# Optimization experiments

Measured on AMD Instinct MI355X. Metric: run time of the kernel, lower is better.

Reference implementation:

```python
import jax, jax.numpy as jnp
import numpy as np

N_NODES = 50000
N_EDGES = 600000
D_IN = 128
HIDDEN = 128
N_CLASSES = 2
BN_EPS = 1e-5


def setup_inputs() -> dict:
    key = jax.random.key(0)
    ks = jax.random.split(key, 10)
    x = jax.random.normal(ks[0], (N_NODES, D_IN), dtype=jnp.float32)
    edge_index = jax.random.randint(ks[1], (2, N_EDGES), 0, N_NODES, dtype=jnp.int64)
    # weights stored [in, out] (transpose of torch Linear.weight)
    s1 = 1.0 / np.sqrt(D_IN)
    s2 = 1.0 / np.sqrt(HIDDEN)
    W1 = jax.random.uniform(ks[2], (D_IN, HIDDEN), jnp.float32, -s1, s1)
    b1 = jax.random.uniform(ks[3], (HIDDEN,), jnp.float32, -s1, s1)
    gamma = jnp.ones((HIDDEN,), jnp.float32)
    beta = jnp.zeros((HIDDEN,), jnp.float32)
    W2 = jax.random.uniform(ks[4], (HIDDEN, HIDDEN), jnp.float32, -s2, s2)
    b2 = jax.random.uniform(ks[5], (HIDDEN,), jnp.float32, -s2, s2)
    Wl = jax.random.uniform(ks[6], (HIDDEN, N_CLASSES), jnp.float32, -s2, s2)
    bl = jax.random.uniform(ks[7], (N_CLASSES,), jnp.float32, -s2, s2)
    return {"x": x, "edge_index": edge_index, "W1": W1, "b1": b1,
            "gamma": gamma, "beta": beta, "W2": W2, "b2": b2,
            "Wl": Wl, "bl": bl}


def reference(x, edge_index, W1, b1, gamma, beta, W2, b2, Wl, bl):
    src, dst = edge_index[0], edge_index[1]
    # GINConv with eps=0 (PyG default): h_i = MLP(x_i + sum_{j->i} x_j)
    agg = jax.ops.segment_sum(x[src], dst, num_segments=N_NODES)  # [N, D]
    h = x + agg
    # MLP: Linear -> ReLU -> BatchNorm1d (train-mode batch stats) -> Linear
    h = jax.nn.relu(h @ W1 + b1)
    mean = jnp.mean(h, axis=0)
    var = jnp.var(h, axis=0)
    h = (h - mean) * jax.lax.rsqrt(var + BN_EPS) * gamma + beta
    h = h @ W2 + b2
    # classifier head
    return h @ Wl + bl  # [N, num_classes]
```

## Files before the change

### kernel.cpp

```cpp
#include <hip/hip_runtime.h>
#include <cstdint>

#define NN 50000
#define NE 600000
#define D 128
#define NPAD 50176
#define NWAVE 3125
#define NBLK 782
#define BS 48
#define NB 196
#define PCAP 4608
#define FA 147
#define WB1 16
#define XB4 782
#define NREP 8

typedef __attribute__((ext_vector_type(8))) short short8;
typedef __attribute__((ext_vector_type(4))) float f32x4;

static __device__ __forceinline__ unsigned short f2bf(float f) {
  unsigned int u = __float_as_uint(f);
  unsigned int r = (u + 0x7FFFu + ((u >> 16) & 1u)) >> 16;
  return (unsigned short)r;
}

__global__ __launch_bounds__(256) void k_prep(const float* __restrict__ x,
                                              const float* __restrict__ W1,
                                              const float* __restrict__ W2,
                                              const float* __restrict__ Wl,
                                              const float* __restrict__ b2,
                                              const float* __restrict__ bl,
                                              const int* __restrict__ ei,
                                              unsigned short* __restrict__ xb,
                                              unsigned short* __restrict__ W1p,
                                              float* __restrict__ Cf,
                                              float* __restrict__ KBf,
                                              int* __restrict__ gcnt,
                                              unsigned* __restrict__ pairs) {
  __shared__ int histA[NB], baseA[NB], curA[NB];
  int blk = blockIdx.x, t = threadIdx.x;
  if (blk < FA) {
    if (t < NB) histA[t] = 0;
    __syncthreads();
    int e0 = blk * 4096 + t;
#pragma unroll
    for (int i = 0; i < 16; ++i) {
      int e = e0 + i * 256;
      if (e < NE) atomicAdd(&histA[ei[NE + e] >> 8], 1);
    }
    __syncthreads();
    if (t < NB) {
      int h = histA[t];
      baseA[t] = h ? atomicAdd(&gcnt[t], h) : 0;
      curA[t] = 0;
    }
    __syncthreads();
#pragma unroll
    for (int i = 0; i < 16; ++i) {
      int e = e0 + i * 256;
      if (e < NE) {
        int s = ei[e];
        int d = ei[NE + e];
        int b = d >> 8;
        int p = baseA[b] + atomicAdd(&curA[b], 1);
        if (p < PCAP) pairs[b * PCAP + p] = (unsigned)s | ((unsigned)(d & 255) << 16);
      }
    }
    return;
  }
  blk -= FA;
  if (blk < WB1) {
    int base = blk * 1024 + t;
#pragma unroll
    for (int i = 0; i < 4; ++i) {
      int rem = base + i * 256;
      int ks = rem >> 12;
      int nf = (rem >> 9) & 7;
      int l  = (rem >> 3) & 63;
      int j  = rem & 7;
      int k = ks * 32 + (l >> 4) * 8 + j;
      int n = nf * 16 + (l & 15);
      W1p[rem] = f2bf(W1[k * D + n]);
    }
    return;
  }
  blk -= WB1;
  if (blk == 0) {
    {
      int k = t >> 1, c = t & 1;
      const float4* w2r = (const float4*)(W2 + k * D);
      float s = 0.f;
#pragma unroll
      for (int m4 = 0; m4 < 32; ++m4) {
        float4 wv = w2r[m4];
        int m = m4 * 4;
        s += wv.x * Wl[(m + 0) * 2 + c] + wv.y * Wl[(m + 1) * 2 + c] +
             wv.z * Wl[(m + 2) * 2 + c] + wv.w * Wl[(m + 3) * 2 + c];
      }
      Cf[k * 2 + c] = s;
    }
    if (t < 2) {
      float s = bl[t];
      for (int m = 0; m < D; ++m) s += b2[m] * Wl[m * 2 + t];
      KBf[t] = s;
    }
    return;
  }
  blk -= 1;
  {
    int64_t base = (int64_t)blk * 1024 + t;
    const float4* xs = (const float4*)x;
#pragma unroll
    for (int i = 0; i < 4; ++i) {
      int64_t idx = base + i * 256;
      if (idx < (int64_t)NN * D / 8) {
        float4 f0 = xs[idx * 2], f1 = xs[idx * 2 + 1];
        uint4 o;
        o.x = (unsigned)f2bf(f0.x) | ((unsigned)f2bf(f0.y) << 16);
        o.y = (unsigned)f2bf(f0.z) | ((unsigned)f2bf(f0.w) << 16);
        o.z = (unsigned)f2bf(f1.x) | ((unsigned)f2bf(f1.y) << 16);
        o.w = (unsigned)f2bf(f1.z) | ((unsigned)f2bf(f1.w) << 16);
        ((uint4*)xb)[idx] = o;
      }
    }
  }
}

__global__ __launch_bounds__(256) void k_fill2(const unsigned* __restrict__ pairs,
                                               const int* __restrict__ gcnt,
                                               unsigned short* __restrict__ colw,
                                               int* __restrict__ cursor) {
  __shared__ unsigned short cs[256 * BS];
  __shared__ int cur[256];
  int b = blockIdx.x, t = threadIdx.x;
  cur[t] = 0;
  __syncthreads();
  int cnt = gcnt[b]; if (cnt > PCAP) cnt = PCAP;
  for (int i = t; i < cnt; i += 256) {
    unsigned u = pairs[b * PCAP + i];
    int dl = (u >> 16) & 255;
    int pos = atomicAdd(&cur[dl], 1);
    if (pos < BS) cs[dl * BS + pos] = (unsigned short)(u & 0xFFFFu);
  }
  __syncthreads();
  uint4* dst = (uint4*)(colw + (size_t)b * 256 * BS);
  const uint4* src = (const uint4*)cs;
  for (int i = t; i < 1536; i += 256) dst[i] = src[i];
  cursor[b * 256 + t] = (cur[t] < BS) ? cur[t] : BS;
}

__global__ __launch_bounds__(256) void k_fusedA(const unsigned short* __restrict__ xb,
                                                const int* __restrict__ cursor,
                                                const unsigned short* __restrict__ colw,
                                                const unsigned short* __restrict__ W1p,
                                                const float* __restrict__ b1,
                                                unsigned short* __restrict__ h1b,
                                                float* __restrict__ stats) {
  __shared__ uint4 tile[64 * 16];
  __shared__ float redS[D], redQ[D];
  int t = threadIdx.x;
  if (t < D) { redS[t] = 0.f; redQ[t] = 0.f; }
  __syncthreads();

  int w = t >> 6, lane = t & 63;
  int g = lane >> 4, l = lane & 15;
  int wave_id = blockIdx.x * 4 + w;
  bool valid = wave_id < NWAVE;
  int row0 = wave_id * 16;
  const uint4* xv = (const uint4*)xb;

  if (valid) {
    int curAll = (lane < 16) ? cursor[row0 + lane] : 0;
#define GSRC(k) __shfl(((k) < 16 ? cl0 : ((k) < 32 ? cl1 : cl2)), (g << 4) + ((k) & 15))
#define MSK(v, kk) { unsigned m_ = ((kk) < dcap) ? 0xFFFFFFFFu : 0u; \
                     (v).x &= m_; (v).y &= m_; (v).z &= m_; (v).w &= m_; }
#define ACC8(v)                                     \
  { a0 += __uint_as_float((v).x << 16);             \
    a1 += __uint_as_float((v).x & 0xFFFF0000u);     \
    a2 += __uint_as_float((v).y << 16);             \
    a3 += __uint_as_float((v).y & 0xFFFF0000u);     \
    a4 += __uint_as_float((v).z << 16);             \
    a5 += __uint_as_float((v).z & 0xFFFF0000u);     \
    a6 += __uint_as_float((v).w << 16);             \
    a7 += __uint_as_float((v).w & 0xFFFF0000u); }
    for (int sub = 0; sub < 4; ++sub) {
      int node = row0 + sub * 4 + g;
      int ec = __shfl(curAll, sub * 4 + g);
      if (ec > BS - 1) ec = BS - 1;
      int dcap = ec + 1;
      int cbase = node * BS;
      int cl0 = (l < ec) ? (int)colw[cbase + l]
                         : ((l == ec) ? node : 0);
      int cl1 = (l + 16 < ec) ? (int)colw[cbase + 16 + l]
                              : ((l + 16 == ec) ? node : 0);
      int cl2 = (l + 32 < ec) ? (int)colw[cbase + 32 + l]
                              : ((l + 32 == ec) ? node : 0);
      int maxd = dcap;
      maxd = max(maxd, __shfl_xor(maxd, 16));
      maxd = max(maxd, __shfl_xor(maxd, 32));
      float a0 = 0, a1 = 0, a2 = 0, a3 = 0, a4 = 0, a5 = 0, a6 = 0, a7 = 0;
      int nit = (maxd + 7) >> 3;
      for (int it = 0; it < nit; ++it) {
        int k0 = it << 3;
        int i0 = GSRC(k0);
        int i1 = GSRC(k0 + 1);
        int i2 = GSRC(k0 + 2);
        int i3 = GSRC(k0 + 3);
        int i4 = GSRC(k0 + 4);
        int i5 = GSRC(k0 + 5);
        int i6 = GSRC(k0 + 6);
        int i7 = GSRC(k0 + 7);
        uint4 v0 = xv[(unsigned)i0 * 16u + l];
        uint4 v1 = xv[(unsigned)i1 * 16u + l];
        uint4 v2 = xv[(unsigned)i2 * 16u + l];
        uint4 v3 = xv[(unsigned)i3 * 16u + l];
        uint4 v4 = xv[(unsigned)i4 * 16u + l];
        uint4 v5 = xv[(unsigned)i5 * 16u + l];
        uint4 v6 = xv[(unsigned)i6 * 16u + l];
        uint4 v7 = xv[(unsigned)i7 * 16u + l];
        MSK(v0, k0) MSK(v1, k0 + 1) MSK(v2, k0 + 2) MSK(v3, k0 + 3)
        MSK(v4, k0 + 4) MSK(v5, k0 + 5) MSK(v6, k0 + 6) MSK(v7, k0 + 7)
        ACC8(v0) ACC8(v1) ACC8(v2) ACC8(v3)
        ACC8(v4) ACC8(v5) ACC8(v6) ACC8(v7)
      }
      uint4 o;
      o.x = (unsigned)f2bf(a0) | ((unsigned)f2bf(a1) << 16);
      o.y = (unsigned)f2bf(a2) | ((unsigned)f2bf(a3) << 16);
      o.z = (unsigned)f2bf(a4) | ((unsigned)f2bf(a5) << 16);
      o.w = (unsigned)f2bf(a6) | ((unsigned)f2bf(a7) << 16);
      int rb = (w << 4) + (sub << 2) + g;
      tile[(rb * 16 + l) ^ (rb & 7)] = o;
    }
#undef GSRC
#undef MSK
#undef ACC8

    {
      int rb = (w << 4) + l;
      short8 a[4];
#pragma unroll
      for (int ks = 0; ks < 4; ++ks)
        a[ks] = *(const short8*)&tile[(rb * 16 + ks * 4 + g) ^ (rb & 7)];

      f32x4 acc[8];
#pragma unroll
      for (int nf = 0; nf < 8; ++nf) { f32x4 z = {0.f, 0.f, 0.f, 0.f}; acc[nf] = z; }

      const short8* B = (const short8*)W1p;
#pragma unroll
      for (int ks = 0; ks < 4; ++ks)
#pragma unroll
        for (int nf = 0; nf < 8; ++nf)
          acc[nf] = __builtin_amdgcn_mfma_f32_16x16x32_bf16(a[ks], B[(ks * 8 + nf) * 64 + lane],
                                                            acc[nf], 0, 0, 0);

#pragma unroll
      for (int nf = 0; nf < 8; ++nf) {
        int colc = nf * 16 + l;
        float bias = b1[colc];
        float ps = 0.f, pq = 0.f;
#pragma unroll
        for (int r = 0; r < 4; ++r) {
          float v = fmaxf(acc[nf][r] + bias, 0.f);
          int row = row0 + g * 4 + r;
          h1b[(int64_t)row * D + colc] = f2bf(v);
          ps += v; pq += v * v;
        }
        ps += __shfl_xor(ps, 16); ps += __shfl_xor(ps, 32);
        pq += __shfl_xor(pq, 16); pq += __shfl_xor(pq, 32);
        if (g == 0) { atomicAdd(&redS[colc], ps); atomicAdd(&redQ[colc], pq); }
      }
    }
  }
  __syncthreads();
  {
    int r = blockIdx.x & (NREP - 1);
    if (t < D) {
      unsafeAtomicAdd(&stats[r * 256 + t], redS[t]);
      unsafeAtomicAdd(&stats[r * 256 + D + t], redQ[t]);
    }
  }
}

__global__ __launch_bounds__(256) void k_head(const unsigned short* __restrict__ h1b,
                                              const float* __restrict__ stats,
                                              const float* __restrict__ gamma,
                                              const float* __restrict__ beta,
                                              const float* __restrict__ Cf,
                                              const float* __restrict__ KBf,
                                              float* __restrict__ out) {
  __shared__ float sc_s[D], sh_s[D];
  __shared__ float2 c2_s[D];
  int t = threadIdx.x;
  if (t < D) {
    float s = 0.f, q = 0.f;
#pragma unroll
    for (int r = 0; r < NREP; ++r) {
      s += stats[r * 256 + t];
      q += stats[r * 256 + D + t];
    }
    const float inv_n = 1.0f / (float)NN;
    float mean = s * inv_n;
    float var = q * inv_n - mean * mean;
    float sc = gamma[t] * rsqrtf(var + 1e-5f);
    sc_s[t] = sc;
    sh_s[t] = beta[t] - mean * sc;
    c2_s[t] = ((const float2*)Cf)[t];
  }
  __syncthreads();
  int node = blockIdx.x * 16 + (t >> 4);
  int l = t & 15;
  uint4 v = ((const uint4*)h1b)[node * 16 + l];
  int k0 = l * 8;
  float e0 = __uint_as_float(v.x << 16), e1 = __uint_as_float(v.x & 0xFFFF0000u);
  float e2 = __uint_as_float(v.y << 16), e3 = __uint_as_float(v.y & 0xFFFF0000u);
  float e4 = __uint_as_float(v.z << 16), e5 = __uint_as_float(v.z & 0xFFFF0000u);
  float e6 = __uint_as_float(v.w << 16), e7 = __uint_as_float(v.w & 0xFFFF0000u);
  float p0 = 0.f, p1 = 0.f;
#define HC(ej, jj) { float u_ = ej * sc_s[k0 + jj] + sh_s[k0 + jj];  \
                     float2 c_ = c2_s[k0 + jj];                      \
                     p0 += u_ * c_.x; p1 += u_ * c_.y; }
  HC(e0, 0) HC(e1, 1) HC(e2, 2) HC(e3, 3) HC(e4, 4) HC(e5, 5) HC(e6, 6) HC(e7, 7)
#undef HC
  p0 += __shfl_xor(p0, 1); p0 += __shfl_xor(p0, 2);
  p0 += __shfl_xor(p0, 4); p0 += __shfl_xor(p0, 8);
  p1 += __shfl_xor(p1, 1); p1 += __shfl_xor(p1, 2);
  p1 += __shfl_xor(p1, 4); p1 += __shfl_xor(p1, 8);
  if (l == 0) {
    float2 kb = ((const float2*)KBf)[0];
    ((float2*)out)[node] = make_float2(p0 + kb.x, p1 + kb.y);
  }
}

extern "C" void kernel_launch(void* const* d_in, const int* in_sizes, int n_in,
                              void* d_out, int out_size, void* d_ws, size_t ws_size,
                              hipStream_t stream) {
  const float* x     = (const float*)d_in[0];
  const int*   ei    = (const int*)d_in[1];
  const float* W1    = (const float*)d_in[2];
  const float* b1    = (const float*)d_in[3];
  const float* gamma = (const float*)d_in[4];
  const float* beta  = (const float*)d_in[5];
  const float* W2    = (const float*)d_in[6];
  const float* b2    = (const float*)d_in[7];
  const float* Wl    = (const float*)d_in[8];
  const float* bl    = (const float*)d_in[9];
  float* out = (float*)d_out;

  unsigned short* xb  = (unsigned short*)d_ws;
  unsigned short* h1b = xb + (int64_t)NN * D;
  unsigned short* W1p = h1b + (int64_t)NN * D;
  float* Cf     = (float*)(W1p + 16384);
  float* KBf    = Cf + 256;
  float* stats  = KBf + 4;
  int* gcnt     = (int*)(stats + NREP * 256);
  int* cursor   = gcnt + 256;
  unsigned* pairs = (unsigned*)(cursor + NPAD);
  unsigned short* colw = (unsigned short*)(pairs + (size_t)NB * PCAP);

  hipMemsetAsync(stats, 0, (NREP * 256 + 256) * sizeof(float), stream);
  k_prep<<<FA + WB1 + 1 + XB4, 256, 0, stream>>>(x, W1, W2, Wl, b2, bl, ei,
                                                 xb, W1p, Cf, KBf, gcnt, pairs);
  k_fill2<<<NB, 256, 0, stream>>>(pairs, gcnt, colw, cursor);
  k_fusedA<<<NBLK, 256, 0, stream>>>(xb, cursor, colw, W1p, b1, h1b, stats);
  k_head<<<NN / 16, 256, 0, stream>>>(h1b, stats, gamma, beta, Cf, KBf, out);
}
```

Baseline: 75.20 us.

## Fuse CSR bucket fill into aggregation kernel and batch head rows per block

Removes the k_fill2 kernel. Each aggregation block now scans its 256-node bucket of (src,dst) pairs itself and builds its 64-node column lists in shared memory, which drops a launch and the global colw/cursor write and read. Each bucket is scanned four times, once by each of the four blocks that share it, and the per-node list cap drops from 48 to 47 entries. The head kernel now processes 64 nodes per block over 782 blocks instead of 3125, and NREP is doubled, apparently to spread the stats atomics over more slots.

Measured after the change: 73.33 us. 2.5% less time.

```diff
diff --git a/kernel.cpp b/kernel.cpp
--- a/kernel.cpp
+++ b/kernel.cpp
@@ -4,7 +4,6 @@
 #define NN 50000
 #define NE 600000
 #define D 128
-#define NPAD 50176
 #define NWAVE 3125
 #define NBLK 782
 #define BS 48
@@ -13,7 +12,7 @@
 #define FA 147
 #define WB1 16
 #define XB4 782
-#define NREP 8
+#define NREP 16
 
 typedef __attribute__((ext_vector_type(8))) short short8;
 typedef __attribute__((ext_vector_type(4))) float f32x4;
@@ -126,40 +125,35 @@
   }
 }
 
-__global__ __launch_bounds__(256) void k_fill2(const unsigned* __restrict__ pairs,
-                                               const int* __restrict__ gcnt,
-                                               unsigned short* __restrict__ colw,
-                                               int* __restrict__ cursor) {
-  __shared__ unsigned short cs[256 * BS];
-  __shared__ int cur[256];
-  int b = blockIdx.x, t = threadIdx.x;
-  cur[t] = 0;
-  __syncthreads();
-  int cnt = gcnt[b]; if (cnt > PCAP) cnt = PCAP;
-  for (int i = t; i < cnt; i += 256) {
-    unsigned u = pairs[b * PCAP + i];
-    int dl = (u >> 16) & 255;
-    int pos = atomicAdd(&cur[dl], 1);
-    if (pos < BS) cs[dl * BS + pos] = (unsigned short)(u & 0xFFFFu);
-  }
-  __syncthreads();
-  uint4* dst = (uint4*)(colw + (size_t)b * 256 * BS);
-  const uint4* src = (const uint4*)cs;
-  for (int i = t; i < 1536; i += 256) dst[i] = src[i];
-  cursor[b * 256 + t] = (cur[t] < BS) ? cur[t] : BS;
-}
-
 __global__ __launch_bounds__(256) void k_fusedA(const unsigned short* __restrict__ xb,
-                                                const int* __restrict__ cursor,
-                                                const unsigned short* __restrict__ colw,
+                                                const int* __restrict__ gcnt,
+                                                const unsigned* __restrict__ pairs,
                                                 const unsigned short* __restrict__ W1p,
                                                 const float* __restrict__ b1,
                                                 unsigned short* __restrict__ h1b,
                                                 float* __restrict__ stats) {
   __shared__ uint4 tile[64 * 16];
+  __shared__ unsigned short cs[64 * BS];
+  __shared__ int cur[64];
   __shared__ float redS[D], redQ[D];
   int t = threadIdx.x;
   if (t < D) { redS[t] = 0.f; redQ[t] = 0.f; }
+  if (t < 64) cur[t] = 0;
+  __syncthreads();
+
+  {
+    int bkt = blockIdx.x >> 2, qt = blockIdx.x & 3;
+    int cnt = gcnt[bkt]; if (cnt > PCAP) cnt = PCAP;
+    for (int i = t; i < cnt; i += 256) {
+      unsigned u = pairs[bkt * PCAP + i];
+      int dloc = (u >> 16) & 255;
+      if ((dloc >> 6) == qt) {
+        int dl = dloc & 63;
+        int pos = atomicAdd(&cur[dl], 1);
+        if (pos < BS - 1) cs[dl * BS + pos] = (unsigned short)(u & 0xFFFFu);
+      }
+    }
+  }
   __syncthreads();
 
   int w = t >> 6, lane = t & 63;
@@ -170,7 +164,6 @@
   const uint4* xv = (const uint4*)xb;
 
   if (valid) {
-    int curAll = (lane < 16) ? cursor[row0 + lane] : 0;
 #define GSRC(k) __shfl(((k) < 16 ? cl0 : ((k) < 32 ? cl1 : cl2)), (g << 4) + ((k) & 15))
 #define MSK(v, kk) { unsigned m_ = ((kk) < dcap) ? 0xFFFFFFFFu : 0u; \
                      (v).x &= m_; (v).y &= m_; (v).z &= m_; (v).w &= m_; }
@@ -184,16 +177,17 @@
     a6 += __uint_as_float((v).w << 16);             \
     a7 += __uint_as_float((v).w & 0xFFFF0000u); }
     for (int sub = 0; sub < 4; ++sub) {
-      int node = row0 + sub * 4 + g;
-      int ec = __shfl(curAll, sub * 4 + g);
+      int dl = (w << 4) + (sub << 2) + g;
+      int node = blockIdx.x * 64 + dl;
+      int ec = cur[dl];
       if (ec > BS - 1) ec = BS - 1;
       int dcap = ec + 1;
-      int cbase = node * BS;
-      int cl0 = (l < ec) ? (int)colw[cbase + l]
+      int cbase = dl * BS;
+      int cl0 = (l < ec) ? (int)cs[cbase + l]
                          : ((l == ec) ? node : 0);
-      int cl1 = (l + 16 < ec) ? (int)colw[cbase + 16 + l]
+      int cl1 = (l + 16 < ec) ? (int)cs[cbase + 16 + l]
                               : ((l + 16 == ec) ? node : 0);
-      int cl2 = (l + 32 < ec) ? (int)colw[cbase + 32 + l]
+      int cl2 = (l + 32 < ec) ? (int)cs[cbase + 32 + l]
                               : ((l + 32 == ec) ? node : 0);
       int maxd = dcap;
       maxd = max(maxd, __shfl_xor(maxd, 16));
@@ -228,8 +222,7 @@
       o.y = (unsigned)f2bf(a2) | ((unsigned)f2bf(a3) << 16);
       o.z = (unsigned)f2bf(a4) | ((unsigned)f2bf(a5) << 16);
       o.w = (unsigned)f2bf(a6) | ((unsigned)f2bf(a7) << 16);
-      int rb = (w << 4) + (sub << 2) + g;
-      tile[(rb * 16 + l) ^ (rb & 7)] = o;
+      tile[(dl * 16 + l) ^ (dl & 7)] = o;
     }
 #undef GSRC
 #undef MSK
@@ -308,27 +301,30 @@
     c2_s[t] = ((const float2*)Cf)[t];
   }
   __syncthreads();
-  int node = blockIdx.x * 16 + (t >> 4);
+  float2 kb = ((const float2*)KBf)[0];
   int l = t & 15;
-  uint4 v = ((const uint4*)h1b)[node * 16 + l];
   int k0 = l * 8;
-  float e0 = __uint_as_float(v.x << 16), e1 = __uint_as_float(v.x & 0xFFFF0000u);
-  float e2 = __uint_as_float(v.y << 16), e3 = __uint_as_float(v.y & 0xFFFF0000u);
-  float e4 = __uint_as_float(v.z << 16), e5 = __uint_as_float(v.z & 0xFFFF0000u);
-  float e6 = __uint_as_float(v.w << 16), e7 = __uint_as_float(v.w & 0xFFFF0000u);
-  float p0 = 0.f, p1 = 0.f;
+#pragma unroll
+  for (int rd = 0; rd < 4; ++rd) {
+    int node = blockIdx.x * 64 + rd * 16 + (t >> 4);
+    if (node < NN) {
+      uint4 v = ((const uint4*)h1b)[(int64_t)node * 16 + l];
+      float e0 = __uint_as_float(v.x << 16), e1 = __uint_as_float(v.x & 0xFFFF0000u);
+      float e2 = __uint_as_float(v.y << 16), e3 = __uint_as_float(v.y & 0xFFFF0000u);
+      float e4 = __uint_as_float(v.z << 16), e5 = __uint_as_float(v.z & 0xFFFF0000u);
+      float e6 = __uint_as_float(v.w << 16), e7 = __uint_as_float(v.w & 0xFFFF0000u);
+      float p0 = 0.f, p1 = 0.f;
 #define HC(ej, jj) { float u_ = ej * sc_s[k0 + jj] + sh_s[k0 + jj];  \
                      float2 c_ = c2_s[k0 + jj];                      \
                      p0 += u_ * c_.x; p1 += u_ * c_.y; }
-  HC(e0, 0) HC(e1, 1) HC(e2, 2) HC(e3, 3) HC(e4, 4) HC(e5, 5) HC(e6, 6) HC(e7, 7)
+      HC(e0, 0) HC(e1, 1) HC(e2, 2) HC(e3, 3) HC(e4, 4) HC(e5, 5) HC(e6, 6) HC(e7, 7)
 #undef HC
-  p0 += __shfl_xor(p0, 1); p0 += __shfl_xor(p0, 2);
-  p0 += __shfl_xor(p0, 4); p0 += __shfl_xor(p0, 8);
-  p1 += __shfl_xor(p1, 1); p1 += __shfl_xor(p1, 2);
-  p1 += __shfl_xor(p1, 4); p1 += __shfl_xor(p1, 8);
-  if (l == 0) {
-    float2 kb = ((const float2*)KBf)[0];
-    ((float2*)out)[node] = make_float2(p0 + kb.x, p1 + kb.y);
+      p0 += __shfl_xor(p0, 1); p0 += __shfl_xor(p0, 2);
+      p0 += __shfl_xor(p0, 4); p0 += __shfl_xor(p0, 8);
+      p1 += __shfl_xor(p1, 1); p1 += __shfl_xor(p1, 2);
+      p1 += __shfl_xor(p1, 4); p1 += __shfl_xor(p1, 8);
+      if (l == 0) ((float2*)out)[node] = make_float2(p0 + kb.x, p1 + kb.y);
+    }
   }
 }
 
@@ -354,14 +350,11 @@
   float* KBf    = Cf + 256;
   float* stats  = KBf + 4;
   int* gcnt     = (int*)(stats + NREP * 256);
-  int* cursor   = gcnt + 256;
-  unsigned* pairs = (unsigned*)(cursor + NPAD);
-  unsigned short* colw = (unsigned short*)(pairs + (size_t)NB * PCAP);
+  unsigned* pairs = (unsigned*)(gcnt + 256);
 
   hipMemsetAsync(stats, 0, (NREP * 256 + 256) * sizeof(float), stream);
   k_prep<<<FA + WB1 + 1 + XB4, 256, 0, stream>>>(x, W1, W2, Wl, b2, bl, ei,
                                                  xb, W1p, Cf, KBf, gcnt, pairs);
-  k_fill2<<<NB, 256, 0, stream>>>(pairs, gcnt, colw, cursor);
-  k_fusedA<<<NBLK, 256, 0, stream>>>(xb, cursor, colw, W1p, b1, h1b, stats);
-  k_head<<<NN / 16, 256, 0, stream>>>(h1b, stats, gamma, beta, Cf, KBf, out);
-}
+  k_fusedA<<<NBLK, 256, 0, stream>>>(xb, gcnt, pairs, W1p, b1, h1b, stats);
+  k_head<<<NBLK, 256, 0, stream>>>(h1b, stats, gamma, beta, Cf, KBf, out);
+}
```
